# Performance work log

Hardware: AMD Instinct MI355X
Metric: run time of the kernel (lower is better)

The kernel has to match this reference:

```python
import jax, jax.numpy as jnp
import numpy as np

N = 2_097_152
TABLE = 32768  # hash table size (power of 2 -> mod == & 32767)
FEAT = 16
H = 64


def setup_inputs() -> dict:
    key = jax.random.key(0)
    k = jax.random.split(key, 9)
    pos = jax.random.normal(k[0], (N, 3), dtype=jnp.float32)
    normal = jax.random.normal(k[1], (N, 3), dtype=jnp.float32)
    emb = jax.random.normal(k[2], (TABLE, FEAT), dtype=jnp.float32) * 0.05
    W1 = jax.random.normal(k[3], (FEAT + 3, H), dtype=jnp.float32) * 0.1
    b1 = jnp.zeros((H,), jnp.float32)
    W2 = jax.random.normal(k[4], (H, H), dtype=jnp.float32) * 0.1
    b2 = jnp.zeros((H,), jnp.float32)
    W3 = jax.random.normal(k[5], (H, 3), dtype=jnp.float32) * 0.1
    b3 = jnp.zeros((3,), jnp.float32)
    return {"pos": pos, "normal": normal, "emb": emb,
            "W1": W1, "b1": b1, "W2": W2, "b2": b2, "W3": W3, "b3": b3}


def _hash_idx(pos):
    # torch .long() truncates toward zero; astype(int32) does the same.
    # Products only matter mod 2^15, so int32 wraparound is safe.
    s = (pos * 8.0).astype(jnp.int32)
    h = (s[:, 0] * np.int32(73856093)) ^ (s[:, 1] * np.int32(19349663)) ^ (s[:, 2] * np.int32(83492791))
    return h & np.int32(TABLE - 1)  # floor-mod by 2^15 == bitwise AND


def reference(pos, normal, emb, W1, b1, W2, b2, W3, b3):
    idx = _hash_idx(pos)                    # [N] int32
    feat = emb[idx]                         # [N,16] gather
    x = jnp.concatenate([feat, normal], axis=-1)  # [N,19]
    h1 = jax.nn.relu(x @ W1 + b1)           # [N,64]
    h2 = jax.nn.relu(h1 @ W2 + b2)          # [N,64]
    return jax.nn.sigmoid(h2 @ W3 + b3)     # [N,3]
```

## Files before the change

kernel.cpp:

```cpp
#include <hip/hip_runtime.h>
#include <cstdint>


typedef short  bf16x8 __attribute__((ext_vector_type(8)));
typedef float  f32x4  __attribute__((ext_vector_type(4)));

#define MFMA16(A, B, C) __builtin_amdgcn_mfma_f32_16x16x32_bf16((A), (B), (C), 0, 0, 0)

__device__ inline int pk(float a, float b) {
    int d;
    __asm__("v_cvt_pk_bf16_f32 %0, %1, %2" : "=v"(d) : "v"(a), "v"(b));
    return d;
}

__device__ inline void pl32_swap(int& a, int& b) {
    __asm__ volatile("v_permlane32_swap_b32 %0, %1" : "+v"(a), "+v"(b));
}
__device__ inline void pl16_swap(int& a, int& b) {
    __asm__ volatile("v_permlane16_swap_b32 %0, %1" : "+v"(a), "+v"(b));
}

__device__ inline void cfence() { __asm__ volatile("" ::: "memory"); }

__device__ inline float sigmoid_fast(float x) {
    float e = __expf(-x);
    return __builtin_amdgcn_rcpf(1.0f + e);
}

__device__ inline void cd_to_frag(const f32x4 acc[4], int4& lo, int4& hi) {
    int P0 = pk(fmaxf(acc[0][0],0.f), fmaxf(acc[0][1],0.f));
    int P1 = pk(fmaxf(acc[0][2],0.f), fmaxf(acc[0][3],0.f));
    int P2 = pk(fmaxf(acc[1][0],0.f), fmaxf(acc[1][1],0.f));
    int P3 = pk(fmaxf(acc[1][2],0.f), fmaxf(acc[1][3],0.f));
    int P4 = pk(fmaxf(acc[2][0],0.f), fmaxf(acc[2][1],0.f));
    int P5 = pk(fmaxf(acc[2][2],0.f), fmaxf(acc[2][3],0.f));
    int P6 = pk(fmaxf(acc[3][0],0.f), fmaxf(acc[3][1],0.f));
    int P7 = pk(fmaxf(acc[3][2],0.f), fmaxf(acc[3][3],0.f));
    pl32_swap(P0, P2); pl16_swap(P0, P2);
    pl32_swap(P1, P3); pl16_swap(P1, P3);
    pl32_swap(P4, P6); pl16_swap(P4, P6);
    pl32_swap(P5, P7); pl16_swap(P5, P7);
    lo = make_int4(P0, P1, P2, P3);
    hi = make_int4(P4, P5, P6, P7);
}

__device__ inline bf16x8 as_frag(int4 v) {
    bf16x8 f; __builtin_memcpy(&f, &v, sizeof(f)); return f;
}

#define XS 40

__global__ __launch_bounds__(256) void nrad_setup_kernel(
    const float* __restrict__ W1, const float* __restrict__ b1,
    const float* __restrict__ W2, const float* __restrict__ W3,
    float* __restrict__ ws)
{
    const int tid  = threadIdx.x;
    const int wv   = tid >> 6;
    const int lane = tid & 63;
    const int q    = lane >> 4;
    const int nn   = lane & 15;
    int4* w1o = (int4*)ws;
    int4* w2o = (int4*)ws + 256;
    int4* w3o = (int4*)ws + 768;

    if (wv == 0) {
        for (int t = 0; t < 4; ++t) {
            int n = t * 16 + nn;
            float v[8];
            #pragma unroll
            for (int j = 0; j < 8; ++j) {
                int k = q * 8 + j;
                v[j] = (k < 19) ? W1[k * 64 + n] : (k == 19 ? b1[n] : 0.0f);
            }
            w1o[t * 64 + lane] = make_int4(pk(v[0],v[1]), pk(v[2],v[3]),
                                           pk(v[4],v[5]), pk(v[6],v[7]));
        }
    } else if (wv == 3) {
        for (int h = 0; h < 2; ++h) {
            float v[8];
            #pragma unroll
            for (int j = 0; j < 8; ++j) {
                int k = h * 32 + q * 8 + j;
                v[j] = (nn < 3) ? W3[k * 3 + nn] : 0.0f;
            }
            w3o[h * 64 + lane] = make_int4(pk(v[0],v[1]), pk(v[2],v[3]),
                                           pk(v[4],v[5]), pk(v[6],v[7]));
        }
    } else {
        for (int tt = 0; tt < 2; ++tt) {
            int t = (wv - 1) * 2 + tt;
            int n = t * 16 + nn;
            for (int ks = 0; ks < 2; ++ks) {
                float v[8];
                #pragma unroll
                for (int j = 0; j < 8; ++j) {
                    int k = ks * 32 + q * 8 + j;
                    v[j] = W2[k * 64 + n];
                }
                w2o[(t * 2 + ks) * 64 + lane] = make_int4(pk(v[0],v[1]), pk(v[2],v[3]),
                                                          pk(v[4],v[5]), pk(v[6],v[7]));
            }
        }
    }
}

__global__ __launch_bounds__(256, 3) void nrad_mfma_kernel(
    const float* __restrict__ pos, const float* __restrict__ nrm,
    const float* __restrict__ emb,
    const float* __restrict__ b2, const float* __restrict__ b3,
    const float* __restrict__ ws, float* __restrict__ out, int ntiles)
{
    __shared__ alignas(16) int4  w2lds[512];
    __shared__ alignas(16) short xbuf[4][64 * XS];

    const int tid  = threadIdx.x;
    const int wave = tid >> 6;
    const int lane = tid & 63;
    const int q    = lane >> 4;
    const int nn   = lane & 15;

    const int4* wsf = (const int4*)ws;
    w2lds[tid]       = wsf[256 + tid];
    w2lds[tid + 256] = wsf[512 + tid];
    __syncthreads();

    bf16x8 w1f[4], w3f[2];
    #pragma unroll
    for (int t = 0; t < 4; ++t) w1f[t] = as_frag(wsf[t * 64 + lane]);
    w3f[0] = as_frag(wsf[768 + lane]);
    w3f[1] = as_frag(wsf[832 + lane]);
    f32x4 b2rv[4];
    #pragma unroll
    for (int t = 0; t < 4; ++t) b2rv[t] = *(const f32x4*)(b2 + t * 16 + q * 4);
    const float b3r = (nn < 3) ? b3[nn] : 0.0f;

    short* xw = &xbuf[wave][0];
    const int4* w2l = w2lds + lane;
    const int xro  = nn * XS + q * 8;
    const int oofs = q * 12 + nn;

    const int wave_gid = blockIdx.x * 4 + wave;
    const int nwaves   = gridDim.x * 4;
    const float4* emb4 = (const float4*)emb;

    for (int tile = wave_gid; tile < ntiles; tile += nwaves) {
        const int base = tile * 64;
        const int i    = base + lane;

        const float* pp = pos + 3 * i;
        const float* np = nrm + 3 * i;
        float p0 = pp[0], p1 = pp[1], p2 = pp[2];
        float n0 = np[0], n1 = np[1], n2 = np[2];
        int s0 = (int)(p0 * 8.0f), s1 = (int)(p1 * 8.0f), s2 = (int)(p2 * 8.0f);
        uint32_t h = ((uint32_t)s0 * 73856093u) ^ ((uint32_t)s1 * 19349663u) ^
                     ((uint32_t)s2 * 83492791u);
        uint32_t idx = h & 32767u;
        float4 f0 = emb4[idx*4+0], f1 = emb4[idx*4+1];
        float4 f2 = emb4[idx*4+2], f3 = emb4[idx*4+3];

        int4 A = make_int4(pk(f0.x, f0.y), pk(f0.z, f0.w), pk(f1.x, f1.y), pk(f1.z, f1.w));
        int4 B = make_int4(pk(f2.x, f2.y), pk(f2.z, f2.w), pk(f3.x, f3.y), pk(f3.z, f3.w));
        int4 C = make_int4(pk(n0, n1), pk(n2, 1.0f), 0, 0);
        int4 D = make_int4(0, 0, 0, 0);
        int4* xr = (int4*)(xw + lane * XS);
        xr[0] = A; xr[1] = B; xr[2] = C; xr[3] = D;
        cfence();

        const float* ob = out + (size_t)base * 3;
        const f32x4 z = {0.0f, 0.0f, 0.0f, 0.0f};

        #pragma unroll
        for (int sp = 0; sp < 2; ++sp) {
            bf16x8 xfA = *(const bf16x8*)(xw + (2*sp)     * 16 * XS + xro);
            bf16x8 xfB = *(const bf16x8*)(xw + (2*sp + 1) * 16 * XS + xro);

            f32x4 a1A[4], a1B[4];
            #pragma unroll
            for (int t = 0; t < 4; ++t) a1A[t] = MFMA16(w1f[t], xfA, z);
            #pragma unroll
            for (int t = 0; t < 4; ++t) a1B[t] = MFMA16(w1f[t], xfB, z);

            int4 lA, hA, lB, hB;
            cd_to_frag(a1A, lA, hA);
            cd_to_frag(a1B, lB, hB);
            bf16x8 h1A0 = as_frag(lA), h1A1 = as_frag(hA);
            bf16x8 h1B0 = as_frag(lB), h1B1 = as_frag(hB);

            f32x4 a2A[4], a2B[4];
            #pragma unroll
            for (int t = 0; t < 4; ++t) {
                bf16x8 w20 = as_frag(w2l[(t * 2 + 0) * 64]);
                bf16x8 w21 = as_frag(w2l[(t * 2 + 1) * 64]);
                f32x4 cA = MFMA16(w20, h1A0, b2rv[t]);
                a2A[t]   = MFMA16(w21, h1A1, cA);
                f32x4 cB = MFMA16(w20, h1B0, b2rv[t]);
                a2B[t]   = MFMA16(w21, h1B1, cB);
            }

            cd_to_frag(a2A, lA, hA);
            cd_to_frag(a2B, lB, hB);
            bf16x8 h2A0 = as_frag(lA), h2A1 = as_frag(hA);
            bf16x8 h2B0 = as_frag(lB), h2B1 = as_frag(hB);

            f32x4 cb = {b3r, b3r, b3r, b3r};
            f32x4 acc3A = MFMA16(h2A1, w3f[1], MFMA16(h2A0, w3f[0], cb));
            f32x4 acc3B = MFMA16(h2B1, w3f[1], MFMA16(h2B0, w3f[0], cb));

            float oA0 = sigmoid_fast(acc3A[0]), oA1 = sigmoid_fast(acc3A[1]);
            float oA2 = sigmoid_fast(acc3A[2]), oA3 = sigmoid_fast(acc3A[3]);
            float oB0 = sigmoid_fast(acc3B[0]), oB1 = sigmoid_fast(acc3B[1]);
            float oB2 = sigmoid_fast(acc3B[2]), oB3 = sigmoid_fast(acc3B[3]);
            if (nn < 3) {
                float* oa = (float*)(ob + (2*sp)     * 48 + oofs);
                float* obp= (float*)(ob + (2*sp + 1) * 48 + oofs);
                oa[0] = oA0; oa[3] = oA1; oa[6] = oA2; oa[9] = oA3;
                obp[0] = oB0; obp[3] = oB1; obp[6] = oB2; obp[9] = oB3;
            }
        }
        cfence();
    }
}

extern "C" void kernel_launch(void* const* d_in, const int* in_sizes, int n_in,
                              void* d_out, int out_size, void* d_ws, size_t ws_size,
                              hipStream_t stream) {
    const float* pos = (const float*)d_in[0];
    const float* nrm = (const float*)d_in[1];
    const float* emb = (const float*)d_in[2];
    const float* W1  = (const float*)d_in[3];
    const float* b1  = (const float*)d_in[4];
    const float* W2  = (const float*)d_in[5];
    const float* b2  = (const float*)d_in[6];
    const float* W3  = (const float*)d_in[7];
    const float* b3  = (const float*)d_in[8];
    float* out = (float*)d_out;
    float* ws  = (float*)d_ws;

    int n = in_sizes[0] / 3;
    int ntiles = n / 64;

    nrad_setup_kernel<<<1, 256, 0, stream>>>(W1, b1, W2, W3, ws);
    nrad_mfma_kernel<<<2048, 256, 0, stream>>>(pos, nrm, emb, b2, b3, ws,
                                               out, ntiles);
}
```

Measured before the change: 144.6 us.

## Prefetch next tile's inputs and fold permlane shuffles into weight row permutation

The per-tile loop now loads the next tile's pos and normal before the MLP work, and issues the embedding gather between the two sub-tile halves, so global latency overlaps with MFMA compute. It also drops the permlane32/16 swaps that rearranged layer activations into MFMA fragment order. Instead, the rows of W2 and W3 are permuted in the setup kernel through a fixed index map, so the accumulator layout can be fed straight into the next MFMA. The cost is more live registers to hold the prefetched data, which may lower occupancy, and correctness now depends on the permutation exactly matching the fragment layout.

```diff
diff --git a/kernel.cpp b/kernel.cpp
--- a/kernel.cpp
+++ b/kernel.cpp
@@ -13,13 +13,6 @@
     return d;
 }
 
-__device__ inline void pl32_swap(int& a, int& b) {
-    __asm__ volatile("v_permlane32_swap_b32 %0, %1" : "+v"(a), "+v"(b));
-}
-__device__ inline void pl16_swap(int& a, int& b) {
-    __asm__ volatile("v_permlane16_swap_b32 %0, %1" : "+v"(a), "+v"(b));
-}
-
 __device__ inline void cfence() { __asm__ volatile("" ::: "memory"); }
 
 __device__ inline float sigmoid_fast(float x) {
@@ -27,21 +20,19 @@
     return __builtin_amdgcn_rcpf(1.0f + e);
 }
 
-__device__ inline void cd_to_frag(const f32x4 acc[4], int4& lo, int4& hi) {
-    int P0 = pk(fmaxf(acc[0][0],0.f), fmaxf(acc[0][1],0.f));
-    int P1 = pk(fmaxf(acc[0][2],0.f), fmaxf(acc[0][3],0.f));
-    int P2 = pk(fmaxf(acc[1][0],0.f), fmaxf(acc[1][1],0.f));
-    int P3 = pk(fmaxf(acc[1][2],0.f), fmaxf(acc[1][3],0.f));
-    int P4 = pk(fmaxf(acc[2][0],0.f), fmaxf(acc[2][1],0.f));
-    int P5 = pk(fmaxf(acc[2][2],0.f), fmaxf(acc[2][3],0.f));
-    int P6 = pk(fmaxf(acc[3][0],0.f), fmaxf(acc[3][1],0.f));
-    int P7 = pk(fmaxf(acc[3][2],0.f), fmaxf(acc[3][3],0.f));
-    pl32_swap(P0, P2); pl16_swap(P0, P2);
-    pl32_swap(P1, P3); pl16_swap(P1, P3);
-    pl32_swap(P4, P6); pl16_swap(P4, P6);
-    pl32_swap(P5, P7); pl16_swap(P5, P7);
-    lo = make_int4(P0, P1, P2, P3);
-    hi = make_int4(P4, P5, P6, P7);
+__device__ inline int lam(int k) {
+    return 32 * (k >> 5) + 16 * ((k >> 2) & 1) + 4 * ((k >> 3) & 3) + (k & 3);
+}
+
+__device__ inline void cd_pack(const f32x4 acc[4], int4& lo, int4& hi) {
+    lo = make_int4(pk(fmaxf(acc[0][0],0.f), fmaxf(acc[0][1],0.f)),
+                   pk(fmaxf(acc[0][2],0.f), fmaxf(acc[0][3],0.f)),
+                   pk(fmaxf(acc[1][0],0.f), fmaxf(acc[1][1],0.f)),
+                   pk(fmaxf(acc[1][2],0.f), fmaxf(acc[1][3],0.f)));
+    hi = make_int4(pk(fmaxf(acc[2][0],0.f), fmaxf(acc[2][1],0.f)),
+                   pk(fmaxf(acc[2][2],0.f), fmaxf(acc[2][3],0.f)),
+                   pk(fmaxf(acc[3][0],0.f), fmaxf(acc[3][1],0.f)),
+                   pk(fmaxf(acc[3][2],0.f), fmaxf(acc[3][3],0.f)));
 }
 
 __device__ inline bf16x8 as_frag(int4 v) {
@@ -81,8 +72,8 @@
             float v[8];
             #pragma unroll
             for (int j = 0; j < 8; ++j) {
-                int k = h * 32 + q * 8 + j;
-                v[j] = (nn < 3) ? W3[k * 3 + nn] : 0.0f;
+                int kin = lam(h * 32 + q * 8 + j);
+                v[j] = (nn < 3) ? W3[kin * 3 + nn] : 0.0f;
             }
             w3o[h * 64 + lane] = make_int4(pk(v[0],v[1]), pk(v[2],v[3]),
                                            pk(v[4],v[5]), pk(v[6],v[7]));
@@ -95,8 +86,8 @@
                 float v[8];
                 #pragma unroll
                 for (int j = 0; j < 8; ++j) {
-                    int k = ks * 32 + q * 8 + j;
-                    v[j] = W2[k * 64 + n];
+                    int kin = lam(ks * 32 + q * 8 + j);
+                    v[j] = W2[kin * 64 + n];
                 }
                 w2o[(t * 2 + ks) * 64 + lane] = make_int4(pk(v[0],v[1]), pk(v[2],v[3]),
                                                           pk(v[4],v[5]), pk(v[6],v[7]));
@@ -144,34 +135,42 @@
     const int nwaves   = gridDim.x * 4;
     const float4* emb4 = (const float4*)emb;
 
-    for (int tile = wave_gid; tile < ntiles; tile += nwaves) {
-        const int base = tile * 64;
-        const int i    = base + lane;
-
-        const float* pp = pos + 3 * i;
-        const float* np = nrm + 3 * i;
-        float p0 = pp[0], p1 = pp[1], p2 = pp[2];
-        float n0 = np[0], n1 = np[1], n2 = np[2];
+    float n0 = 0, n1 = 0, n2 = 0;
+    float4 f0{}, f1{}, f2{}, f3{};
+    if (wave_gid < ntiles) {
+        int i = wave_gid * 64 + lane;
+        float p0 = pos[3*i], p1 = pos[3*i+1], p2 = pos[3*i+2];
+        n0 = nrm[3*i]; n1 = nrm[3*i+1]; n2 = nrm[3*i+2];
         int s0 = (int)(p0 * 8.0f), s1 = (int)(p1 * 8.0f), s2 = (int)(p2 * 8.0f);
         uint32_t h = ((uint32_t)s0 * 73856093u) ^ ((uint32_t)s1 * 19349663u) ^
                      ((uint32_t)s2 * 83492791u);
         uint32_t idx = h & 32767u;
-        float4 f0 = emb4[idx*4+0], f1 = emb4[idx*4+1];
-        float4 f2 = emb4[idx*4+2], f3 = emb4[idx*4+3];
-
-        int4 A = make_int4(pk(f0.x, f0.y), pk(f0.z, f0.w), pk(f1.x, f1.y), pk(f1.z, f1.w));
-        int4 B = make_int4(pk(f2.x, f2.y), pk(f2.z, f2.w), pk(f3.x, f3.y), pk(f3.z, f3.w));
-        int4 C = make_int4(pk(n0, n1), pk(n2, 1.0f), 0, 0);
-        int4 D = make_int4(0, 0, 0, 0);
-        int4* xr = (int4*)(xw + lane * XS);
-        xr[0] = A; xr[1] = B; xr[2] = C; xr[3] = D;
-        cfence();
-
+        f0 = emb4[idx*4+0]; f1 = emb4[idx*4+1];
+        f2 = emb4[idx*4+2]; f3 = emb4[idx*4+3];
+    }
+
+    for (int tile = wave_gid; tile < ntiles; tile += nwaves) {
+        const int base = tile * 64;
         const float* ob = out + (size_t)base * 3;
         const f32x4 z = {0.0f, 0.0f, 0.0f, 0.0f};
 
-        #pragma unroll
-        for (int sp = 0; sp < 2; ++sp) {
+        {
+            int4 A = make_int4(pk(f0.x, f0.y), pk(f0.z, f0.w), pk(f1.x, f1.y), pk(f1.z, f1.w));
+            int4 B = make_int4(pk(f2.x, f2.y), pk(f2.z, f2.w), pk(f3.x, f3.y), pk(f3.z, f3.w));
+            int4 C = make_int4(pk(n0, n1), pk(n2, 1.0f), 0, 0);
+            int4 D = make_int4(0, 0, 0, 0);
+            int4* xr = (int4*)(xw + lane * XS);
+            xr[0] = A; xr[1] = B; xr[2] = C; xr[3] = D;
+        }
+        cfence();
+
+        int nt = tile + nwaves;
+        int lt = (nt < ntiles) ? nt : tile;
+        int inext = lt * 64 + lane;
+        float q0 = pos[3*inext], q1 = pos[3*inext+1], q2 = pos[3*inext+2];
+        n0 = nrm[3*inext]; n1 = nrm[3*inext+1]; n2 = nrm[3*inext+2];
+
+        auto do_pair = [&](int sp) {
             bf16x8 xfA = *(const bf16x8*)(xw + (2*sp)     * 16 * XS + xro);
             bf16x8 xfB = *(const bf16x8*)(xw + (2*sp + 1) * 16 * XS + xro);
 
@@ -182,8 +181,8 @@
             for (int t = 0; t < 4; ++t) a1B[t] = MFMA16(w1f[t], xfB, z);
 
             int4 lA, hA, lB, hB;
-            cd_to_frag(a1A, lA, hA);
-            cd_to_frag(a1B, lB, hB);
+            cd_pack(a1A, lA, hA);
+            cd_pack(a1B, lB, hB);
             bf16x8 h1A0 = as_frag(lA), h1A1 = as_frag(hA);
             bf16x8 h1B0 = as_frag(lB), h1B1 = as_frag(hB);
 
@@ -198,8 +197,8 @@
                 a2B[t]   = MFMA16(w21, h1B1, cB);
             }
 
-            cd_to_frag(a2A, lA, hA);
-            cd_to_frag(a2B, lB, hB);
+            cd_pack(a2A, lA, hA);
+            cd_pack(a2B, lB, hB);
             bf16x8 h2A0 = as_frag(lA), h2A1 = as_frag(hA);
             bf16x8 h2B0 = as_frag(lB), h2B1 = as_frag(hB);
 
@@ -217,7 +216,21 @@
                 oa[0] = oA0; oa[3] = oA1; oa[6] = oA2; oa[9] = oA3;
                 obp[0] = oB0; obp[3] = oB1; obp[6] = oB2; obp[9] = oB3;
             }
-        }
+        };
+
+        do_pair(0);
+
+        {
+            int s0 = (int)(q0 * 8.0f), s1 = (int)(q1 * 8.0f), s2 = (int)(q2 * 8.0f);
+            uint32_t h = ((uint32_t)s0 * 73856093u) ^ ((uint32_t)s1 * 19349663u) ^
+                         ((uint32_t)s2 * 83492791u);
+            uint32_t idx = h & 32767u;
+            f0 = emb4[idx*4+0]; f1 = emb4[idx*4+1];
+            f2 = emb4[idx*4+2]; f3 = emb4[idx*4+3];
+        }
+
+        do_pair(1);
+
         cfence();
     }
 }
```

Result: no change. 142.1 us (-1.7%).
